# Kernel optimization log

Measured on AMD Instinct MI355X. Metric: run time of the kernel, lower is better.

The kernel has to match this reference:

```python
import jax, jax.numpy as jnp
import numpy as np

DIM = 768
DIM_QKV = 64
NUM_HEAD = 12
EPS = 1e-5


def layer_norm(x, gamma, beta):
    mu = jnp.mean(x, axis=-1, keepdims=True)
    var = jnp.mean(jnp.square(x - mu), axis=-1, keepdims=True)
    return (x - mu) * jax.lax.rsqrt(var + EPS) * gamma + beta


def setup_inputs() -> dict:
    key = jax.random.key(0)
    ks = jax.random.split(key, 10)
    s = 0.02
    x = jax.random.normal(ks[0], (4, 2048, DIM), dtype=jnp.float32)
    wq = jax.random.normal(ks[1], (DIM, DIM_QKV), dtype=jnp.float32) * s
    wk = jax.random.normal(ks[2], (DIM, DIM_QKV), dtype=jnp.float32) * s
    wv = jax.random.normal(ks[3], (DIM, DIM_QKV), dtype=jnp.float32) * s
    lin_w = jax.random.normal(ks[4], (DIM_QKV * NUM_HEAD, DIM), dtype=jnp.float32) * s
    lin_b = jnp.zeros((DIM,), dtype=jnp.float32)
    ln1_g = jnp.ones((DIM,), dtype=jnp.float32)
    ln1_b = jnp.zeros((DIM,), dtype=jnp.float32)
    fc1_w = jax.random.normal(ks[5], (DIM, 4 * DIM), dtype=jnp.float32) * s
    fc1_b = jnp.zeros((4 * DIM,), dtype=jnp.float32)
    fc2_w = jax.random.normal(ks[6], (4 * DIM, DIM), dtype=jnp.float32) * s
    fc2_b = jnp.zeros((DIM,), dtype=jnp.float32)
    return {"x": x, "wq": wq, "wk": wk, "wv": wv, "lin_w": lin_w,
            "lin_b": lin_b, "ln1_g": ln1_g, "ln1_b": ln1_b,
            "fc1_w": fc1_w, "fc1_b": fc1_b, "fc2_w": fc2_w, "fc2_b": fc2_b}


def reference(x, wq, wk, wv, lin_w, lin_b, ln1_g, ln1_b, fc1_w, fc1_b, fc2_w, fc2_b):
    identity1 = x
    h = layer_norm(x, ln1_g, ln1_b)
    # single shared-weight attention head (original calls the same module num_head times)
    q = h @ wq  # [B,S,Dq]
    k = h @ wk
    v = h @ wv
    scores = jnp.einsum('bik,bjk->bij', q, k) / (DIM_QKV ** 0.5)  # [B,S,S]
    attn = jax.nn.softmax(scores, axis=-1)
    out_head = attn @ v  # [B,S,Dq]
    # concat of num_head identical outputs == tile along last dim
    cat = jnp.tile(out_head, (1, 1, NUM_HEAD))  # [B,S,Dq*H]
    attn_out = cat @ lin_w + lin_b
    out = attn_out + identity1
    identity2 = out
    # NOTE: original reuses layer_norm_1 here (layer_norm_2 is unused)
    out = layer_norm(out, ln1_g, ln1_b)
    out = jax.nn.gelu(out @ fc1_w + fc1_b, approximate=False)
    out = out @ fc2_w + fc2_b
    return out + identity2
```

## Files before the change

kernel.cpp:

```cpp
#include <hip/hip_runtime.h>

typedef unsigned short u16;
typedef unsigned int u32;
typedef __bf16 bf16x8 __attribute__((ext_vector_type(8)));
typedef float f32x4 __attribute__((ext_vector_type(4)));

__device__ __forceinline__ u16 f2bf(float f) {
  u32 u = __float_as_uint(f);
  u32 r = (u + 0x7FFFu + ((u >> 16) & 1u)) >> 16;
  return (u16)r;
}

__device__ __forceinline__ float gelu_exact(float x) {
  return 0.5f * x * (1.f + erff(x * 0.70710678118654752f));
}

__global__ void transpose_cast(const float* __restrict__ in, u16* __restrict__ out,
                               int R, int C) {
  __shared__ float tile[32][33];
  int c0 = blockIdx.x * 32, r0 = blockIdx.y * 32;
  int tx = threadIdx.x, ty = threadIdx.y;
  for (int i = 0; i < 32; i += 8) {
    int r = r0 + ty + i, c = c0 + tx;
    tile[ty + i][tx] = (r < R && c < C) ? in[(long)r * C + c] : 0.f;
  }
  __syncthreads();
  for (int i = 0; i < 32; i += 8) {
    int oc = c0 + ty + i, orr = r0 + tx;
    if (oc < C && orr < R) out[(long)oc * R + orr] = f2bf(tile[tx][ty + i]);
  }
}

__global__ void weff_build(const float* __restrict__ lin_w, u16* __restrict__ weffT) {
  int idx = blockIdx.x * 256 + threadIdx.x;
  if (idx >= 768 * 64) return;
  int n = idx % 768, d = idx / 768;
  float s = 0.f;
#pragma unroll
  for (int j = 0; j < 12; j++) s += lin_w[(long)(j * 64 + d) * 768 + n];
  weffT[(long)n * 64 + d] = f2bf(s);
}

__global__ __launch_bounds__(256)
void ln_rows(const float* __restrict__ in, const float* __restrict__ gamma,
             const float* __restrict__ beta, u16* __restrict__ out, int nrows) {
  int gid = blockIdx.x * blockDim.x + threadIdx.x;
  int wid = gid >> 6, l = gid & 63;
  if (wid >= nrows) return;
  const float4* row = (const float4*)(in + (long)wid * 768);
  float4 v[3];
  float s = 0.f, s2 = 0.f;
#pragma unroll
  for (int j = 0; j < 3; j++) {
    v[j] = row[l + 64 * j];
    s += v[j].x + v[j].y + v[j].z + v[j].w;
    s2 += v[j].x * v[j].x + v[j].y * v[j].y + v[j].z * v[j].z + v[j].w * v[j].w;
  }
#pragma unroll
  for (int off = 1; off < 64; off <<= 1) {
    s += __shfl_xor(s, off);
    s2 += __shfl_xor(s2, off);
  }
  float mean = s * (1.f / 768.f);
  float rstd = rsqrtf(s2 * (1.f / 768.f) - mean * mean + 1e-5f);
  u16* orow = out + (long)wid * 768;
#pragma unroll
  for (int j = 0; j < 3; j++) {
    float4 g = ((const float4*)gamma)[l + 64 * j];
    float4 b = ((const float4*)beta)[l + 64 * j];
    ushort4 o;
    o.x = f2bf((v[j].x - mean) * rstd * g.x + b.x);
    o.y = f2bf((v[j].y - mean) * rstd * g.y + b.y);
    o.z = f2bf((v[j].z - mean) * rstd * g.z + b.z);
    o.w = f2bf((v[j].w - mean) * rstd * g.w + b.w);
    ((ushort4*)orow)[l + 64 * j] = o;
  }
}

template <int EPI>
__global__ __launch_bounds__(256, 2)
void gemm_bt(const u16* __restrict__ A, const u16* __restrict__ Bt,
             const float* __restrict__ bias, const float* __restrict__ res,
             void* __restrict__ outv, int M, int N, int K, int ldo) {
  __shared__ __align__(16) u16 Alds[128 * 40];
  __shared__ __align__(16) u16 Blds[128 * 40];
  const int t = threadIdx.x;
  const int w = t >> 6, l = t & 63;
  const int wr = w >> 1, wc = w & 1;
  const u16* aptr = A + ((long)(blockIdx.x * 128 + (t >> 2))) * K + (t & 3) * 8;
  const u16* bptr = Bt + ((long)(blockIdx.y * 128 + (t >> 2))) * K + (t & 3) * 8;
  const long step64 = (long)64 * K;
  const int lw0 = (t >> 2) * 40 + (t & 3) * 8;
  const int lw1 = lw0 + 64 * 40;
  const int ar = (wr * 64 + (l & 15)) * 40 + ((l >> 4) * 8);
  const int br = (wc * 64 + (l & 15)) * 40 + ((l >> 4) * 8);
  f32x4 acc[4][4] = {};
  const int ksteps = K >> 5;
  for (int ks = 0; ks < ksteps; ++ks) {
    uint4 a0 = *(const uint4*)(aptr);
    uint4 a1 = *(const uint4*)(aptr + step64);
    uint4 b0 = *(const uint4*)(bptr);
    uint4 b1 = *(const uint4*)(bptr + step64);
    __syncthreads();
    *(uint4*)(&Alds[lw0]) = a0;
    *(uint4*)(&Alds[lw1]) = a1;
    *(uint4*)(&Blds[lw0]) = b0;
    *(uint4*)(&Blds[lw1]) = b1;
    __syncthreads();
    bf16x8 af[4], bfr[4];
#pragma unroll
    for (int i = 0; i < 4; i++) af[i] = *(const bf16x8*)(&Alds[ar + i * 16 * 40]);
#pragma unroll
    for (int i = 0; i < 4; i++) bfr[i] = *(const bf16x8*)(&Blds[br + i * 16 * 40]);
#pragma unroll
    for (int mf = 0; mf < 4; mf++)
#pragma unroll
      for (int nf = 0; nf < 4; nf++)
        acc[mf][nf] = __builtin_amdgcn_mfma_f32_16x16x32_bf16(af[mf], bfr[nf], acc[mf][nf], 0, 0, 0);
    aptr += 32;
    bptr += 32;
  }
  const int rowbase = blockIdx.x * 128 + wr * 64 + ((l >> 4) * 4);
  const int colbase = blockIdx.y * 128 + wc * 64 + (l & 15);
#pragma unroll
  for (int nf = 0; nf < 4; nf++) {
    int col = colbase + nf * 16;
    if (col >= N) continue;
    float bv = (EPI == 0) ? 0.f : bias[col];
#pragma unroll
    for (int mf = 0; mf < 4; mf++) {
#pragma unroll
      for (int i = 0; i < 4; i++) {
        long row = rowbase + mf * 16 + i;
        float v = acc[mf][nf][i] + bv;
        if (EPI == 2) v = gelu_exact(v);
        if (EPI == 1) {
          v += res[row * ldo + col];
          ((float*)outv)[row * ldo + col] = v;
        } else {
          ((u16*)outv)[row * ldo + col] = f2bf(v);
        }
      }
    }
  }
}

__global__ __launch_bounds__(128)
void attn_fwd(const u16* __restrict__ qkv, u16* __restrict__ oh) {
  __shared__ __align__(16) u16 Klds[32 * 72];
  __shared__ __align__(16) u16 Vlds[64 * 40];
  __shared__ __align__(16) u16 Plds[2][16 * 40];
  const int t = threadIdx.x, w = t >> 6, l = t & 63;
  const int r0 = blockIdx.x * 32;
  const long bb = (long)(r0 & ~2047);
  const int qrow = r0 + w * 16 + (l & 15);
  bf16x8 qf0 = *(const bf16x8*)(qkv + (long)qrow * 192 + ((l >> 4) * 8));
  bf16x8 qf1 = *(const bf16x8*)(qkv + (long)qrow * 192 + 32 + ((l >> 4) * 8));
  f32x4 po[4] = {};
  float m_i[4], l_i[4];
#pragma unroll
  for (int i = 0; i < 4; i++) { m_i[i] = -1e30f; l_i[i] = 0.f; }
  const int kkey = t >> 3, kseg = t & 7;
  for (int st = 0; st < 2048; st += 32) {
    uint4 k0 = *(const uint4*)(qkv + (bb + st + kkey) * 192 + 64 + kseg * 8);
    uint4 k1 = *(const uint4*)(qkv + (bb + st + 16 + kkey) * 192 + 64 + kseg * 8);
    u16 vv[16];
#pragma unroll
    for (int i = 0; i < 16; i++) {
      int e = t + 128 * i;
      vv[i] = qkv[(bb + st + (e >> 6)) * 192 + 128 + (e & 63)];
    }
    __syncthreads();
    *(uint4*)(&Klds[kkey * 72 + kseg * 8]) = k0;
    *(uint4*)(&Klds[(16 + kkey) * 72 + kseg * 8]) = k1;
#pragma unroll
    for (int i = 0; i < 16; i++) {
      int e = t + 128 * i;
      Vlds[(e & 63) * 40 + (e >> 6)] = vv[i];
    }
    __syncthreads();
    f32x4 s0 = {}, s1 = {};
    {
      bf16x8 ka = *(const bf16x8*)(&Klds[(l & 15) * 72 + ((l >> 4) * 8)]);
      bf16x8 kb = *(const bf16x8*)(&Klds[(l & 15) * 72 + 32 + ((l >> 4) * 8)]);
      s0 = __builtin_amdgcn_mfma_f32_16x16x32_bf16(qf0, ka, s0, 0, 0, 0);
      s0 = __builtin_amdgcn_mfma_f32_16x16x32_bf16(qf1, kb, s0, 0, 0, 0);
      bf16x8 kc = *(const bf16x8*)(&Klds[(16 + (l & 15)) * 72 + ((l >> 4) * 8)]);
      bf16x8 kd = *(const bf16x8*)(&Klds[(16 + (l & 15)) * 72 + 32 + ((l >> 4) * 8)]);
      s1 = __builtin_amdgcn_mfma_f32_16x16x32_bf16(qf0, kc, s1, 0, 0, 0);
      s1 = __builtin_amdgcn_mfma_f32_16x16x32_bf16(qf1, kd, s1, 0, 0, 0);
    }
    float sf[4];
#pragma unroll
    for (int i = 0; i < 4; i++) {
      float a = s0[i] * 0.125f, b = s1[i] * 0.125f;
      float tm = fmaxf(a, b);
#pragma unroll
      for (int off = 1; off < 16; off <<= 1) tm = fmaxf(tm, __shfl_xor(tm, off));
      float mn = fmaxf(m_i[i], tm);
      sf[i] = __expf(m_i[i] - mn);
      m_i[i] = mn;
      a = __expf(a - mn);
      b = __expf(b - mn);
      float rs = a + b;
#pragma unroll
      for (int off = 1; off < 16; off <<= 1) rs += __shfl_xor(rs, off);
      l_i[i] = l_i[i] * sf[i] + rs;
      int prow = (l >> 4) * 4 + i;
      Plds[w][prow * 40 + (l & 15)] = f2bf(a);
      Plds[w][prow * 40 + 16 + (l & 15)] = f2bf(b);
    }
#pragma unroll
    for (int n = 0; n < 4; n++)
#pragma unroll
      for (int i = 0; i < 4; i++) po[n][i] *= sf[i];
    bf16x8 pf = *(const bf16x8*)(&Plds[w][(l & 15) * 40 + ((l >> 4) * 8)]);
#pragma unroll
    for (int n = 0; n < 4; n++) {
      bf16x8 vf = *(const bf16x8*)(&Vlds[(n * 16 + (l & 15)) * 40 + ((l >> 4) * 8)]);
      po[n] = __builtin_amdgcn_mfma_f32_16x16x32_bf16(pf, vf, po[n], 0, 0, 0);
    }
  }
#pragma unroll
  for (int n = 0; n < 4; n++)
#pragma unroll
    for (int i = 0; i < 4; i++) {
      long row = r0 + w * 16 + ((l >> 4) * 4) + i;
      int feat = n * 16 + (l & 15);
      oh[row * 64 + feat] = f2bf(po[n][i] / l_i[i]);
    }
}

extern "C" void kernel_launch(void* const* d_in, const int* in_sizes, int n_in,
                              void* d_out, int out_size, void* d_ws, size_t ws_size,
                              hipStream_t stream) {
  const float* x = (const float*)d_in[0];
  const float* wq = (const float*)d_in[1];
  const float* wk = (const float*)d_in[2];
  const float* wv = (const float*)d_in[3];
  const float* lin_w = (const float*)d_in[4];
  const float* lin_b = (const float*)d_in[5];
  const float* ln1_g = (const float*)d_in[6];
  const float* ln1_b = (const float*)d_in[7];
  const float* fc1_w = (const float*)d_in[8];
  const float* fc1_b = (const float*)d_in[9];
  const float* fc2_w = (const float*)d_in[10];
  const float* fc2_b = (const float*)d_in[11];
  float* out = (float*)d_out;

  char* p = (char*)d_ws;
  u16* wqkvT = (u16*)p; p += 256 * 768 * 2;
  u16* weffT = (u16*)p; p += 768 * 64 * 2;
  u16* fc1wT = (u16*)p; p += (size_t)3072 * 768 * 2;
  u16* fc2wT = (u16*)p; p += (size_t)768 * 3072 * 2;
  u16* h = (u16*)p; p += (size_t)8192 * 768 * 2;
  u16* qkv = (u16*)p; p += (size_t)8192 * 192 * 2;
  u16* oh = (u16*)p; p += (size_t)8192 * 64 * 2;
  float* out1 = (float*)p; p += (size_t)8192 * 768 * 4;
  u16* a1 = (u16*)p; p += (size_t)8192 * 3072 * 2;

  dim3 tb(32, 8);
  transpose_cast<<<dim3(2, 24), tb, 0, stream>>>(wq, wqkvT, 768, 64);
  transpose_cast<<<dim3(2, 24), tb, 0, stream>>>(wk, wqkvT + 64 * 768, 768, 64);
  transpose_cast<<<dim3(2, 24), tb, 0, stream>>>(wv, wqkvT + 128 * 768, 768, 64);
  hipMemsetAsync(wqkvT + 192 * 768, 0, 64 * 768 * 2, stream);
  transpose_cast<<<dim3(96, 24), tb, 0, stream>>>(fc1_w, fc1wT, 768, 3072);
  transpose_cast<<<dim3(24, 96), tb, 0, stream>>>(fc2_w, fc2wT, 3072, 768);
  weff_build<<<192, 256, 0, stream>>>(lin_w, weffT);

  ln_rows<<<2048, 256, 0, stream>>>(x, ln1_g, ln1_b, h, 8192);
  gemm_bt<0><<<dim3(64, 2), 256, 0, stream>>>(h, wqkvT, nullptr, nullptr, qkv,
                                              8192, 192, 768, 192);
  attn_fwd<<<256, 128, 0, stream>>>(qkv, oh);
  gemm_bt<1><<<dim3(64, 6), 256, 0, stream>>>(oh, weffT, lin_b, x, out1,
                                              8192, 768, 64, 768);
  ln_rows<<<2048, 256, 0, stream>>>(out1, ln1_g, ln1_b, h, 8192);
  gemm_bt<2><<<dim3(64, 24), 256, 0, stream>>>(h, fc1wT, fc1_b, nullptr, a1,
                                               8192, 3072, 768, 3072);
  gemm_bt<1><<<dim3(64, 6), 256, 0, stream>>>(a1, fc2wT, fc2_b, out1, out,
                                              8192, 768, 3072, 768);
}
```

Measured before the change: 379.0 us.

## Split attention over key ranges with merge pass; use direct global-to-LDS loads in GEMM

Attention now splits the 2048 keys into four 512-key chunks across a second grid dimension. Each chunk writes partial outputs plus its row max and row sum to scratch reused from the a1 buffer, and a new merge kernel combines them into oh. This raises the attention grid from 256 to 1024 blocks so the GPU is better filled, at the cost of extra fp32 partial traffic and one more launch. The GEMM also switches to global_load_lds direct-to-LDS loads with an unpadded 32-wide LDS layout, which skips the register staging but may add LDS bank conflicts.

```diff
diff --git a/kernel.cpp b/kernel.cpp
--- a/kernel.cpp
+++ b/kernel.cpp
@@ -13,6 +13,11 @@
 
 __device__ __forceinline__ float gelu_exact(float x) {
   return 0.5f * x * (1.f + erff(x * 0.70710678118654752f));
+}
+
+__device__ __forceinline__ void gload16(const u16* g, u16* l) {
+  __builtin_amdgcn_global_load_lds((const __attribute__((address_space(1))) void*)g,
+                                   (__attribute__((address_space(3))) void*)l, 16, 0, 0);
 }
 
 __global__ void transpose_cast(const float* __restrict__ in, u16* __restrict__ out,
@@ -82,36 +87,34 @@
 void gemm_bt(const u16* __restrict__ A, const u16* __restrict__ Bt,
              const float* __restrict__ bias, const float* __restrict__ res,
              void* __restrict__ outv, int M, int N, int K, int ldo) {
-  __shared__ __align__(16) u16 Alds[128 * 40];
-  __shared__ __align__(16) u16 Blds[128 * 40];
+  __shared__ __align__(16) u16 Alds[128 * 32];
+  __shared__ __align__(16) u16 Blds[128 * 32];
   const int t = threadIdx.x;
   const int w = t >> 6, l = t & 63;
   const int wr = w >> 1, wc = w & 1;
-  const u16* aptr = A + ((long)(blockIdx.x * 128 + (t >> 2))) * K + (t & 3) * 8;
-  const u16* bptr = Bt + ((long)(blockIdx.y * 128 + (t >> 2))) * K + (t & 3) * 8;
-  const long step64 = (long)64 * K;
-  const int lw0 = (t >> 2) * 40 + (t & 3) * 8;
-  const int lw1 = lw0 + 64 * 40;
-  const int ar = (wr * 64 + (l & 15)) * 40 + ((l >> 4) * 8);
-  const int br = (wc * 64 + (l & 15)) * 40 + ((l >> 4) * 8);
+  const int srow = w * 32 + (l >> 2);
+  const int scol = (l & 3) * 8;
+  const u16* aptr = A + (long)(blockIdx.x * 128 + srow) * K + scol;
+  const u16* bptr = Bt + (long)(blockIdx.y * 128 + srow) * K + scol;
+  const long j16 = (long)16 * K;
+  u16* albase = &Alds[(w * 32) * 32];
+  u16* blbase = &Blds[(w * 32) * 32];
+  const int ar = (wr * 64 + (l & 15)) * 32 + (l >> 4) * 8;
+  const int br = (wc * 64 + (l & 15)) * 32 + (l >> 4) * 8;
   f32x4 acc[4][4] = {};
-  const int ksteps = K >> 5;
-  for (int ks = 0; ks < ksteps; ++ks) {
-    uint4 a0 = *(const uint4*)(aptr);
-    uint4 a1 = *(const uint4*)(aptr + step64);
-    uint4 b0 = *(const uint4*)(bptr);
-    uint4 b1 = *(const uint4*)(bptr + step64);
+  for (int ks = 0; ks < K; ks += 32) {
     __syncthreads();
-    *(uint4*)(&Alds[lw0]) = a0;
-    *(uint4*)(&Alds[lw1]) = a1;
-    *(uint4*)(&Blds[lw0]) = b0;
-    *(uint4*)(&Blds[lw1]) = b1;
+    gload16(aptr, albase);
+    gload16(aptr + j16, albase + 16 * 32);
+    gload16(bptr, blbase);
+    gload16(bptr + j16, blbase + 16 * 32);
+    asm volatile("s_waitcnt vmcnt(0)" ::: "memory");
     __syncthreads();
     bf16x8 af[4], bfr[4];
 #pragma unroll
-    for (int i = 0; i < 4; i++) af[i] = *(const bf16x8*)(&Alds[ar + i * 16 * 40]);
-#pragma unroll
-    for (int i = 0; i < 4; i++) bfr[i] = *(const bf16x8*)(&Blds[br + i * 16 * 40]);
+    for (int i = 0; i < 4; i++) af[i] = *(const bf16x8*)(&Alds[ar + i * 16 * 32]);
+#pragma unroll
+    for (int i = 0; i < 4; i++) bfr[i] = *(const bf16x8*)(&Blds[br + i * 16 * 32]);
 #pragma unroll
     for (int mf = 0; mf < 4; mf++)
 #pragma unroll
@@ -146,12 +149,14 @@
 }
 
 __global__ __launch_bounds__(128)
-void attn_fwd(const u16* __restrict__ qkv, u16* __restrict__ oh) {
+void attn_fwd(const u16* __restrict__ qkv, float* __restrict__ pout,
+              float* __restrict__ pm, float* __restrict__ pl) {
   __shared__ __align__(16) u16 Klds[32 * 72];
   __shared__ __align__(16) u16 Vlds[64 * 40];
   __shared__ __align__(16) u16 Plds[2][16 * 40];
   const int t = threadIdx.x, w = t >> 6, l = t & 63;
   const int r0 = blockIdx.x * 32;
+  const int sp = blockIdx.y;
   const long bb = (long)(r0 & ~2047);
   const int qrow = r0 + w * 16 + (l & 15);
   bf16x8 qf0 = *(const bf16x8*)(qkv + (long)qrow * 192 + ((l >> 4) * 8));
@@ -161,7 +166,7 @@
 #pragma unroll
   for (int i = 0; i < 4; i++) { m_i[i] = -1e30f; l_i[i] = 0.f; }
   const int kkey = t >> 3, kseg = t & 7;
-  for (int st = 0; st < 2048; st += 32) {
+  for (int st = sp * 512; st < sp * 512 + 512; st += 32) {
     uint4 k0 = *(const uint4*)(qkv + (bb + st + kkey) * 192 + 64 + kseg * 8);
     uint4 k1 = *(const uint4*)(qkv + (bb + st + 16 + kkey) * 192 + 64 + kseg * 8);
     u16 vv[16];
@@ -222,13 +227,34 @@
     }
   }
 #pragma unroll
-  for (int n = 0; n < 4; n++)
-#pragma unroll
-    for (int i = 0; i < 4; i++) {
-      long row = r0 + w * 16 + ((l >> 4) * 4) + i;
-      int feat = n * 16 + (l & 15);
-      oh[row * 64 + feat] = f2bf(po[n][i] / l_i[i]);
-    }
+  for (int i = 0; i < 4; i++) {
+    long row = r0 + w * 16 + ((l >> 4) * 4) + i;
+    if ((l & 15) == 0) {
+      pm[(long)sp * 8192 + row] = m_i[i];
+      pl[(long)sp * 8192 + row] = l_i[i];
+    }
+#pragma unroll
+    for (int n = 0; n < 4; n++)
+      pout[((long)sp * 8192 + row) * 64 + n * 16 + (l & 15)] = po[n][i];
+  }
+}
+
+__global__ __launch_bounds__(256)
+void attn_merge(const float* __restrict__ pout, const float* __restrict__ pm,
+                const float* __restrict__ pl, u16* __restrict__ oh) {
+  int gid = blockIdx.x * 256 + threadIdx.x;
+  int row = gid >> 6;
+  float M = -1e30f;
+#pragma unroll
+  for (int s = 0; s < 4; s++) M = fmaxf(M, pm[s * 8192 + row]);
+  float L = 0.f, acc = 0.f;
+#pragma unroll
+  for (int s = 0; s < 4; s++) {
+    float e = __expf(pm[s * 8192 + row] - M);
+    L += pl[s * 8192 + row] * e;
+    acc += pout[((long)s * 8192 + row) * 64 + (gid & 63)] * e;
+  }
+  oh[gid] = f2bf(acc / L);
 }
 
 extern "C" void kernel_launch(void* const* d_in, const int* in_sizes, int n_in,
@@ -258,6 +284,9 @@
   u16* oh = (u16*)p; p += (size_t)8192 * 64 * 2;
   float* out1 = (float*)p; p += (size_t)8192 * 768 * 4;
   u16* a1 = (u16*)p; p += (size_t)8192 * 3072 * 2;
+  float* pout = (float*)a1;
+  float* pm = pout + (size_t)4 * 8192 * 64;
+  float* pl = pm + 4 * 8192;
 
   dim3 tb(32, 8);
   transpose_cast<<<dim3(2, 24), tb, 0, stream>>>(wq, wqkvT, 768, 64);
@@ -271,7 +300,8 @@
   ln_rows<<<2048, 256, 0, stream>>>(x, ln1_g, ln1_b, h, 8192);
   gemm_bt<0><<<dim3(64, 2), 256, 0, stream>>>(h, wqkvT, nullptr, nullptr, qkv,
                                               8192, 192, 768, 192);
-  attn_fwd<<<256, 128, 0, stream>>>(qkv, oh);
+  attn_fwd<<<dim3(256, 4), 128, 0, stream>>>(qkv, pout, pm, pl);
+  attn_merge<<<2048, 256, 0, stream>>>(pout, pm, pl, oh);
   gemm_bt<1><<<dim3(64, 6), 256, 0, stream>>>(oh, weffT, lin_b, x, out1,
                                               8192, 768, 64, 768);
   ln_rows<<<2048, 256, 0, stream>>>(out1, ln1_g, ln1_b, h, 8192);
```

Result: faster. 332.8 us (-12.2%).
